# Optimization experiments

Hardware: AMD Instinct MI355X
Metric: run time of the kernel (lower is better)

## Reference

```python
import jax, jax.numpy as jnp
import numpy as np

BN_EPS = 1e-5


def setup_inputs() -> dict:
    key = jax.random.key(0)
    ks = jax.random.split(key, 10)
    N, C, T, V, S, IC = 128, 64, 288, 16, 3, 16
    x = jax.random.normal(ks[0], (N, C, T, V), dtype=jnp.float32)
    A_base = jax.random.uniform(ks[1], (S, V, V), dtype=jnp.float32)
    PA = jax.random.normal(ks[2], (S, V, V), dtype=jnp.float32) * 1e-3
    Wa = jax.random.normal(ks[3], (S, IC, C), dtype=jnp.float32) * 0.1
    ba = jax.random.normal(ks[4], (S, IC), dtype=jnp.float32) * 0.1
    Wb = jax.random.normal(ks[5], (S, IC, C), dtype=jnp.float32) * 0.1
    bb = jax.random.normal(ks[6], (S, IC), dtype=jnp.float32) * 0.1
    Wd = jax.random.normal(ks[7], (S, C, C), dtype=jnp.float32) * 0.1
    bd = jax.random.normal(ks[8], (S, C), dtype=jnp.float32) * 0.1
    gamma = jnp.ones((C,), dtype=jnp.float32)
    beta = jnp.zeros((C,), dtype=jnp.float32)
    return {"x": x, "A_base": A_base, "PA": PA, "Wa": Wa, "ba": ba,
            "Wb": Wb, "bb": bb, "Wd": Wd, "bd": bd,
            "gamma": gamma, "beta": beta}


def reference(x, A_base, PA, Wa, ba, Wb, bb, Wd, bd, gamma, beta):
    N, C, T, V = x.shape
    S, IC, _ = Wa.shape
    A = A_base + PA  # [s,v,w]
    # 1x1 convs for all subsets at once: [n,s,ic,t,v]
    fa = jnp.einsum('nctv,sic->nsitv', x, Wa) + ba[None, :, :, None, None]
    fb = jnp.einsum('nctv,sic->nsitv', x, Wb) + bb[None, :, :, None, None]
    # A1: permute(0,3,1,2).view(N,V,IC*T) -> [n,s,v,(ic*t)]
    A1 = fa.transpose(0, 1, 4, 2, 3).reshape(N, S, V, IC * T)
    # A2: view(N, IC*T, V) -> [n,s,(ic*t),v]
    A2 = fb.reshape(N, S, IC * T, V)
    att = jnp.einsum('nsvk,nskw->nsvw', A1, A2) / float(IC * T)
    att = jax.nn.softmax(att, axis=2)  # torch softmax(dim=1) on [N,V,V]
    att = att + A[None]  # [n,s,v,w]
    # x.view(N,C*T,V) @ att, per subset: [n,s,c,t,w]
    z = jnp.einsum('nctv,nsvw->nsctw', x, att)
    # conv_d per subset then sum over subsets
    y = jnp.einsum('nsctw,soc->notw', z, Wd) + bd.sum(0)[None, :, None, None]
    # inference BN (running mean 0, var 1)
    scale = gamma / jnp.sqrt(1.0 + BN_EPS)
    y = y * scale[None, :, None, None] + beta[None, :, None, None]
    # residual (in_channels == out_channels -> identity down path)
    return y + x
```

## Files before the change

kernel.cpp:

```cpp
#include <hip/hip_runtime.h>
#include <math.h>

#define NN 128
#define CC 64
#define TT 288
#define VV 16
#define SS 3
#define ICC 16

#define SLICES 12
#define TSL (TT / SLICES)
#define CHUNKS (TSL / 8)

#define OTB 16

typedef __attribute__((ext_vector_type(8))) short s16x8;
typedef __attribute__((ext_vector_type(4))) float f32x4;

#define MFMA16(a, b, c) __builtin_amdgcn_mfma_f32_16x16x32_bf16(a, b, c, 0, 0, 0)

__device__ __forceinline__ unsigned short f2bf(float f) {
    union { float f; unsigned u; } x; x.f = f;
    unsigned r = (x.u + 0x7FFFu + ((x.u >> 16) & 1u)) >> 16;
    return (unsigned short)r;
}

__device__ __forceinline__ unsigned cvt2bf(float lo, float hi) {
    unsigned r;
    asm("v_cvt_pk_bf16_f32 %0, %1, %2" : "=v"(r) : "v"(lo), "v"(hi));
    return r;
}

__device__ __forceinline__ s16x8 zero8() {
    s16x8 z;
#pragma unroll
    for (int j = 0; j < 8; ++j) z[j] = 0;
    return z;
}

__device__ __forceinline__ s16x8 cvt8g(const float* p) {
    float4 a = *(const float4*)p;
    float4 b = *(const float4*)(p + 4);
    union { unsigned u[4]; s16x8 v; } r;
    r.u[0] = cvt2bf(a.x, a.y); r.u[1] = cvt2bf(a.z, a.w);
    r.u[2] = cvt2bf(b.x, b.y); r.u[3] = cvt2bf(b.z, b.w);
    return r.v;
}

__device__ __forceinline__ int xaddr(int col, int c) {
    int chunk = ((c >> 3) ^ (col & 7) ^ ((col >> 3) & 7)) & 7;
    return col * 64 + chunk * 8 + (c & 7);
}
__device__ __forceinline__ int xaddr16(int col, int ck) {
    int chunk = (ck ^ (col & 7) ^ ((col >> 3) & 7)) & 7;
    return col * 64 + chunk * 8;
}

__global__ void k_prep(const float* __restrict__ bd, const float* __restrict__ gamma,
                       const float* __restrict__ beta, const float* __restrict__ Wd,
                       float* __restrict__ cmul, float* __restrict__ cadd,
                       unsigned short* __restrict__ wd_bf) {
    const int tid = threadIdx.x;
    if (blockIdx.x == 0 && tid < CC) {
        float mul = gamma[tid] * rsqrtf(1.0f + 1e-5f);
        float add = (bd[tid] + bd[CC + tid] + bd[2 * CC + tid]) * mul + beta[tid];
        cmul[tid] = mul;
        cadd[tid] = add;
    }
    for (int e = blockIdx.x * 256 + tid; e < SS * CC * CC; e += 16 * 256)
        wd_bf[e] = f2bf(Wd[e]);
}

__global__ __launch_bounds__(256) void k_logits(
    const float* __restrict__ x,
    const float* __restrict__ Wa, const float* __restrict__ ba,
    const float* __restrict__ Wb, const float* __restrict__ bb,
    float* __restrict__ part)
{
    const int b    = blockIdx.x;
    const int n    = b / SLICES;
    const int sl   = b % SLICES;
    const int tid  = threadIdx.x;
    const int lane = tid & 63;
    const int wave = tid >> 6;
    const int q    = lane >> 4;
    const int m    = lane & 15;

    __shared__ __align__(16) unsigned short xsb[128 * 64];
    __shared__ __align__(16) unsigned short fa_l[SS][16][136];
    __shared__ __align__(16) unsigned short fb_l[SS][16][136];

    s16x8 wa[SS][2], wb[SS][2];
    float4 ba_r[SS], bb_r[SS];
#pragma unroll
    for (int s = 0; s < SS; ++s) {
#pragma unroll
        for (int kt = 0; kt < 2; ++kt) {
            wa[s][kt] = cvt8g(Wa + ((size_t)(s * ICC + m) * CC + kt * 32 + q * 8));
            wb[s][kt] = cvt8g(Wb + ((size_t)(s * ICC + m) * CC + kt * 32 + q * 8));
        }
        ba_r[s] = *(const float4*)(ba + s * ICC + q * 4);
        bb_r[s] = *(const float4*)(bb + s * ICC + q * 4);
    }

    f32x4 accL[SS];
#pragma unroll
    for (int s = 0; s < SS; ++s)
#pragma unroll
        for (int r = 0; r < 4; ++r) accL[s][r] = 0.0f;

    const float* xn = x + (size_t)n * CC * TT * VV;
    const int tbase = sl * TSL;

    float4 px[8];
#pragma unroll
    for (int i = 0; i < 8; ++i) {
        int f4 = tid + i * 256;
        int c = f4 >> 5, col4 = (f4 & 31) * 4;
        px[i] = *(const float4*)(xn + (size_t)c * (TT * VV) + (size_t)tbase * VV + col4);
    }

#pragma unroll
    for (int ch = 0; ch < CHUNKS; ++ch) {
        __syncthreads();
#pragma unroll
        for (int i = 0; i < 8; ++i) {
            int f4 = tid + i * 256;
            int c = f4 >> 5, col4 = (f4 & 31) * 4;
            unsigned s01 = cvt2bf(px[i].x, px[i].y);
            unsigned s23 = cvt2bf(px[i].z, px[i].w);
            xsb[xaddr(col4 + 0, c)] = (unsigned short)(s01 & 0xffff);
            xsb[xaddr(col4 + 1, c)] = (unsigned short)(s01 >> 16);
            xsb[xaddr(col4 + 2, c)] = (unsigned short)(s23 & 0xffff);
            xsb[xaddr(col4 + 3, c)] = (unsigned short)(s23 >> 16);
        }
        __syncthreads();

        s16x8 bx[2][2];
#pragma unroll
        for (int tli = 0; tli < 2; ++tli) {
            int col = (wave * 2 + tli) * 16 + m;
#pragma unroll
            for (int kt = 0; kt < 2; ++kt)
                bx[tli][kt] = *(const s16x8*)&xsb[xaddr16(col, kt * 4 + q)];
        }

        if (ch + 1 < CHUNKS) {
#pragma unroll
            for (int i = 0; i < 8; ++i) {
                int f4 = tid + i * 256;
                int c = f4 >> 5, col4 = (f4 & 31) * 4;
                px[i] = *(const float4*)(xn + (size_t)c * (TT * VV) +
                                         (size_t)(tbase + (ch + 1) * 8) * VV + col4);
            }
        }

#pragma unroll
        for (int s = 0; s < SS; ++s) {
#pragma unroll
            for (int tli = 0; tli < 2; ++tli) {
                const int tl = wave * 2 + tli;
                f32x4 aa, ab;
                aa[0] = ba_r[s].x; aa[1] = ba_r[s].y; aa[2] = ba_r[s].z; aa[3] = ba_r[s].w;
                ab[0] = bb_r[s].x; ab[1] = bb_r[s].y; ab[2] = bb_r[s].z; ab[3] = bb_r[s].w;
#pragma unroll
                for (int kt = 0; kt < 2; ++kt) {
                    aa = MFMA16(wa[s][kt], bx[tli][kt], aa);
                    ab = MFMA16(wb[s][kt], bx[tli][kt], ab);
                }
                uint2 ua, ub;
                ua.x = cvt2bf(aa[0], aa[1]); ua.y = cvt2bf(aa[2], aa[3]);
                ub.x = cvt2bf(ab[0], ab[1]); ub.y = cvt2bf(ab[2], ab[3]);
                *reinterpret_cast<uint2*>(&fa_l[s][m][tl * 16 + 4 * q]) = ua;
                *reinterpret_cast<uint2*>(&fb_l[s][m][tl * 16 + 4 * q]) = ub;
            }
            s16x8 A2 = *(const s16x8*)&fa_l[s][m][wave * 32 + q * 8];
            s16x8 B2 = *(const s16x8*)&fb_l[s][m][wave * 32 + q * 8];
            accL[s] = MFMA16(A2, B2, accL[s]);
        }
    }

    __syncthreads();
    float* red = (float*)xsb;
#pragma unroll
    for (int s = 0; s < SS; ++s)
#pragma unroll
        for (int r = 0; r < 4; ++r)
            red[(s * 4 + wave) * 256 + (4 * q + r) * 16 + m] = accL[s][r];
    __syncthreads();
#pragma unroll
    for (int s = 0; s < SS; ++s) {
        float v = red[(s * 4 + 0) * 256 + tid] + red[(s * 4 + 1) * 256 + tid] +
                  red[(s * 4 + 2) * 256 + tid] + red[(s * 4 + 3) * 256 + tid];
        part[((size_t)(sl * NN + n) * SS + s) * 256 + tid] = v;
    }
}

__global__ __launch_bounds__(256) void k_softmax(
    const float* __restrict__ part,
    const float* __restrict__ A_base, const float* __restrict__ PA,
    float* __restrict__ att)
{
    const int n = blockIdx.x / SS;
    const int s = blockIdx.x % SS;
    const int tid = threadIdx.x;
    const int w = tid & 15;

    __shared__ float l[256];
    size_t base = ((size_t)n * SS + s) * 256;
    float mine = 0.0f;
#pragma unroll
    for (int p = 0; p < SLICES; ++p)
        mine += part[(size_t)p * (NN * SS * 256) + base + tid];
    mine *= (1.0f / (ICC * TT));
    l[tid] = mine;
    __syncthreads();

    float mx = -1e30f;
#pragma unroll
    for (int v2 = 0; v2 < 16; ++v2) mx = fmaxf(mx, l[v2 * 16 + w]);
    float sm = 0.f;
#pragma unroll
    for (int v2 = 0; v2 < 16; ++v2) sm += __expf(l[v2 * 16 + w] - mx);
    float r = __expf(mine - mx) / sm;

    int aidx = (s * VV * VV) + tid;
    att[base + tid] = r + A_base[aidx] + PA[aidx];
}

__global__ __launch_bounds__(256) void k_out(
    const float* __restrict__ x, const float* __restrict__ att,
    const unsigned short* __restrict__ wd_bf,
    const float* __restrict__ cmul, const float* __restrict__ cadd,
    float* __restrict__ out)
{
    const int b  = blockIdx.x;
    const int n  = b / (TT / OTB);
    const int t0 = (b % (TT / OTB)) * OTB;

    const int tid  = threadIdx.x;
    const int lane = tid & 63;
    const int wave = tid >> 6;
    const int q    = lane >> 4;
    const int m    = lane & 15;

    __shared__ __align__(16) unsigned char uni[36864];
    __shared__ __align__(16) unsigned short attL[SS][16][24];

    unsigned short* xsb = (unsigned short*)uni;
    unsigned short* zsb = (unsigned short*)uni;
    float*          osb = (float*)uni;

    {
        const float* xrow0 = x + ((size_t)(n * CC) * TT + t0) * VV;
#pragma unroll
        for (int i = 0; i < 16; ++i) {
            int c = wave * 16 + i;
            float4 f = *(const float4*)(xrow0 + (size_t)c * (TT * VV) + lane * 4);
            uint2 u2; u2.x = cvt2bf(f.x, f.y); u2.y = cvt2bf(f.z, f.w);
            int tcol  = lane * 4;
            int chunk = (tcol >> 3) ^ (c & 7);
            *(uint2*)&xsb[c * 256 + chunk * 8 + (tcol & 7)] = u2;
        }
    }
    for (int e = tid; e < SS * 256; e += 256) {
        int ss = e >> 8, vv = (e >> 4) & 15, ww = e & 15;
        attL[ss][ww][vv] = f2bf(att[((size_t)n * SS + ss) * 256 + vv * 16 + ww]);
    }

    __syncthreads();

    s16x8 xf[4][4];
#pragma unroll
    for (int cc = 0; cc < 4; ++cc)
#pragma unroll
        for (int u = 0; u < 4; ++u) {
            s16x8 f = zero8();
            if (q < 2) {
                int c = cc * 16 + m;
                int chunk = ((4 * wave + u) * 2 + q) ^ (c & 7);
                f = *(const s16x8*)&xsb[c * 256 + chunk * 8];
            }
            xf[cc][u] = f;
        }

    __syncthreads();

    f32x4 acc[4][4];
#pragma unroll
    for (int p = 0; p < 4; ++p)
#pragma unroll
        for (int u = 0; u < 4; ++u)
#pragma unroll
            for (int r = 0; r < 4; ++r) acc[p][u][r] = 0.0f;

#pragma unroll
    for (int s = 0; s < SS; ++s) {
        s16x8 af = zero8();
        if (q < 2) af = *(const s16x8*)&attL[s][m][q * 8];

#pragma unroll
        for (int u = 0; u < 4; ++u)
#pragma unroll
            for (int cc = 0; cc < 4; ++cc) {
                f32x4 z;
#pragma unroll
                for (int r = 0; r < 4; ++r) z[r] = 0.0f;
                z = MFMA16(xf[cc][u], af, z);
                uint2 uz; uz.x = cvt2bf(z[0], z[1]); uz.y = cvt2bf(z[2], z[3]);
                *(uint2*)&zsb[((wave * 64) + u * 16 + m) * 72 + cc * 16 + 4 * q] = uz;
            }

        s16x8 zf[4][2];
#pragma unroll
        for (int u = 0; u < 4; ++u)
#pragma unroll
            for (int kt = 0; kt < 2; ++kt)
                zf[u][kt] = *(const s16x8*)&zsb[((wave * 64) + u * 16 + m) * 72 +
                                                kt * 32 + q * 8];

#pragma unroll
        for (int p = 0; p < 4; ++p) {
            s16x8 wf[2];
#pragma unroll
            for (int kt = 0; kt < 2; ++kt)
                wf[kt] = *(const s16x8*)(wd_bf +
                           ((size_t)(s * CC + p * 16 + m) * CC + kt * 32 + q * 8));
#pragma unroll
            for (int u = 0; u < 4; ++u)
#pragma unroll
                for (int kt = 0; kt < 2; ++kt)
                    acc[p][u] = MFMA16(wf[kt], zf[u][kt], acc[p][u]);
        }
    }

#pragma unroll
    for (int p = 0; p < 4; ++p) {
        float4 mu = *(const float4*)(cmul + p * 16 + 4 * q);
        float4 ad = *(const float4*)(cadd + p * 16 + 4 * q);
        float mur[4] = {mu.x, mu.y, mu.z, mu.w};
        float adr[4] = {ad.x, ad.y, ad.z, ad.w};
#pragma unroll
        for (int u = 0; u < 4; ++u)
#pragma unroll
            for (int r = 0; r < 4; ++r)
                acc[p][u][r] = acc[p][u][r] * mur[r] + adr[r];
    }

#pragma unroll
    for (int hp = 0; hp < 2; ++hp) {
        __syncthreads();
#pragma unroll
        for (int pp = 0; pp < 2; ++pp)
#pragma unroll
            for (int u = 0; u < 4; ++u)
#pragma unroll
                for (int r = 0; r < 4; ++r)
                    osb[(pp * 16 + 4 * q + r) * 268 + (4 * wave + u) * 16 + m] =
                        acc[hp * 2 + pp][u][r];
        __syncthreads();
#pragma unroll
        for (int j = 0; j < 8; ++j) {
            int orow = wave * 8 + j;
            int o = hp * 32 + orow;
            float4 v = *(const float4*)&osb[orow * 268 + lane * 4];
            size_t off = ((size_t)(n * CC + o) * TT + t0) * VV + lane * 4;
            float4 xr = *(const float4*)(x + off);
            float4 res;
            res.x = v.x + xr.x; res.y = v.y + xr.y;
            res.z = v.z + xr.z; res.w = v.w + xr.w;
            *(float4*)(out + off) = res;
        }
    }
}

extern "C" void kernel_launch(void* const* d_in, const int* in_sizes, int n_in,
                              void* d_out, int out_size, void* d_ws, size_t ws_size,
                              hipStream_t stream) {
    const float* x      = (const float*)d_in[0];
    const float* A_base = (const float*)d_in[1];
    const float* PA     = (const float*)d_in[2];
    const float* Wa     = (const float*)d_in[3];
    const float* ba     = (const float*)d_in[4];
    const float* Wb     = (const float*)d_in[5];
    const float* bb     = (const float*)d_in[6];
    const float* Wd     = (const float*)d_in[7];
    const float* bd     = (const float*)d_in[8];
    const float* gamma  = (const float*)d_in[9];
    const float* beta   = (const float*)d_in[10];
    float* out = (float*)d_out;

    float* part = (float*)d_ws;
    float* att  = part;
    float* cmul = part + (size_t)SLICES * NN * SS * 256;
    float* cadd = cmul + CC;
    unsigned short* wd_bf = (unsigned short*)(cadd + CC);

    k_prep<<<16, 256, 0, stream>>>(bd, gamma, beta, Wd, cmul, cadd, wd_bf);
    k_logits<<<NN * SLICES, 256, 0, stream>>>(x, Wa, ba, Wb, bb, part);
    k_softmax<<<NN * SS, 256, 0, stream>>>(part, A_base, PA, att);
    k_out<<<NN * (TT / OTB), 256, 0, stream>>>(x, att, wd_bf, cmul, cadd, out);
}
```

Measured before the change: 351.9 us.

## Halve output time tile and write k_out results directly with residual from LDS

Shrinks the k_out time tile from 16 to 8 steps, which doubles the number of blocks and halves the per-wave register tiles. xsb and zsb now get separate LDS buffers, so one barrier goes away. The fp32 LDS staging of the output and the second global read of x are dropped. Each lane now writes its MFMA accumulators straight to global memory as scalar stores, adding the residual from the bf16 copy of x held in LDS. This cuts LDS round-trips and global reads, but the stores become narrower and less coalesced, and the residual add now uses bf16-rounded x, which lowers accuracy.

```diff
diff --git a/kernel.cpp b/kernel.cpp
--- a/kernel.cpp
+++ b/kernel.cpp
@@ -12,7 +12,7 @@
 #define TSL (TT / SLICES)
 #define CHUNKS (TSL / 8)
 
-#define OTB 16
+#define OTB 8
 
 typedef __attribute__((ext_vector_type(8))) short s16x8;
 typedef __attribute__((ext_vector_type(4))) float f32x4;
@@ -244,23 +244,21 @@
     const int q    = lane >> 4;
     const int m    = lane & 15;
 
-    __shared__ __align__(16) unsigned char uni[36864];
+    __shared__ __align__(16) unsigned short xsb[64 * 128];
+    __shared__ __align__(16) unsigned short zsb[4 * 32 * 72];
     __shared__ __align__(16) unsigned short attL[SS][16][24];
-
-    unsigned short* xsb = (unsigned short*)uni;
-    unsigned short* zsb = (unsigned short*)uni;
-    float*          osb = (float*)uni;
 
     {
         const float* xrow0 = x + ((size_t)(n * CC) * TT + t0) * VV;
 #pragma unroll
-        for (int i = 0; i < 16; ++i) {
-            int c = wave * 16 + i;
-            float4 f = *(const float4*)(xrow0 + (size_t)c * (TT * VV) + lane * 4);
+        for (int i = 0; i < 8; ++i) {
+            int f4   = tid + i * 256;
+            int c    = f4 >> 5;
+            int col4 = (f4 & 31) * 4;
+            float4 f = *(const float4*)(xrow0 + (size_t)c * (TT * VV) + col4);
             uint2 u2; u2.x = cvt2bf(f.x, f.y); u2.y = cvt2bf(f.z, f.w);
-            int tcol  = lane * 4;
-            int chunk = (tcol >> 3) ^ (c & 7);
-            *(uint2*)&xsb[c * 256 + chunk * 8 + (tcol & 7)] = u2;
+            int chunk = (col4 >> 3) ^ (c & 7);
+            *(uint2*)&xsb[c * 128 + chunk * 8 + (col4 & 7)] = u2;
         }
     }
     for (int e = tid; e < SS * 256; e += 256) {
@@ -270,27 +268,26 @@
 
     __syncthreads();
 
-    s16x8 xf[4][4];
+    s16x8 xf[4][2];
 #pragma unroll
     for (int cc = 0; cc < 4; ++cc)
 #pragma unroll
-        for (int u = 0; u < 4; ++u) {
+        for (int u = 0; u < 2; ++u) {
             s16x8 f = zero8();
             if (q < 2) {
                 int c = cc * 16 + m;
-                int chunk = ((4 * wave + u) * 2 + q) ^ (c & 7);
-                f = *(const s16x8*)&xsb[c * 256 + chunk * 8];
+                int t = wave * 2 + u;
+                int chunk = (2 * t + q) ^ (c & 7);
+                f = *(const s16x8*)&xsb[c * 128 + chunk * 8];
             }
             xf[cc][u] = f;
         }
 
-    __syncthreads();
-
-    f32x4 acc[4][4];
+    f32x4 acc[4][2];
 #pragma unroll
     for (int p = 0; p < 4; ++p)
 #pragma unroll
-        for (int u = 0; u < 4; ++u)
+        for (int u = 0; u < 2; ++u)
 #pragma unroll
             for (int r = 0; r < 4; ++r) acc[p][u][r] = 0.0f;
 
@@ -300,7 +297,7 @@
         if (q < 2) af = *(const s16x8*)&attL[s][m][q * 8];
 
 #pragma unroll
-        for (int u = 0; u < 4; ++u)
+        for (int u = 0; u < 2; ++u)
 #pragma unroll
             for (int cc = 0; cc < 4; ++cc) {
                 f32x4 z;
@@ -308,15 +305,15 @@
                 for (int r = 0; r < 4; ++r) z[r] = 0.0f;
                 z = MFMA16(xf[cc][u], af, z);
                 uint2 uz; uz.x = cvt2bf(z[0], z[1]); uz.y = cvt2bf(z[2], z[3]);
-                *(uint2*)&zsb[((wave * 64) + u * 16 + m) * 72 + cc * 16 + 4 * q] = uz;
-            }
-
-        s16x8 zf[4][2];
-#pragma unroll
-        for (int u = 0; u < 4; ++u)
+                *(uint2*)&zsb[(wave * 32 + u * 16 + m) * 72 + cc * 16 + 4 * q] = uz;
+            }
+
+        s16x8 zf[2][2];
+#pragma unroll
+        for (int u = 0; u < 2; ++u)
 #pragma unroll
             for (int kt = 0; kt < 2; ++kt)
-                zf[u][kt] = *(const s16x8*)&zsb[((wave * 64) + u * 16 + m) * 72 +
+                zf[u][kt] = *(const s16x8*)&zsb[(wave * 32 + u * 16 + m) * 72 +
                                                 kt * 32 + q * 8];
 
 #pragma unroll
@@ -327,13 +324,14 @@
                 wf[kt] = *(const s16x8*)(wd_bf +
                            ((size_t)(s * CC + p * 16 + m) * CC + kt * 32 + q * 8));
 #pragma unroll
-            for (int u = 0; u < 4; ++u)
+            for (int u = 0; u < 2; ++u)
 #pragma unroll
                 for (int kt = 0; kt < 2; ++kt)
                     acc[p][u] = MFMA16(wf[kt], zf[u][kt], acc[p][u]);
         }
     }
 
+    const size_t obase = ((size_t)(n * CC) * TT + t0) * VV;
 #pragma unroll
     for (int p = 0; p < 4; ++p) {
         float4 mu = *(const float4*)(cmul + p * 16 + 4 * q);
@@ -341,35 +339,18 @@
         float mur[4] = {mu.x, mu.y, mu.z, mu.w};
         float adr[4] = {ad.x, ad.y, ad.z, ad.w};
 #pragma unroll
-        for (int u = 0; u < 4; ++u)
-#pragma unroll
-            for (int r = 0; r < 4; ++r)
-                acc[p][u][r] = acc[p][u][r] * mur[r] + adr[r];
-    }
-
-#pragma unroll
-    for (int hp = 0; hp < 2; ++hp) {
-        __syncthreads();
-#pragma unroll
-        for (int pp = 0; pp < 2; ++pp)
-#pragma unroll
-            for (int u = 0; u < 4; ++u)
-#pragma unroll
-                for (int r = 0; r < 4; ++r)
-                    osb[(pp * 16 + 4 * q + r) * 268 + (4 * wave + u) * 16 + m] =
-                        acc[hp * 2 + pp][u][r];
-        __syncthreads();
-#pragma unroll
-        for (int j = 0; j < 8; ++j) {
-            int orow = wave * 8 + j;
-            int o = hp * 32 + orow;
-            float4 v = *(const float4*)&osb[orow * 268 + lane * 4];
-            size_t off = ((size_t)(n * CC + o) * TT + t0) * VV + lane * 4;
-            float4 xr = *(const float4*)(x + off);
-            float4 res;
-            res.x = v.x + xr.x; res.y = v.y + xr.y;
-            res.z = v.z + xr.z; res.w = v.w + xr.w;
-            *(float4*)(out + off) = res;
+        for (int u = 0; u < 2; ++u) {
+            int tl   = wave * 2 + u;
+            int tcol = tl * 16 + m;
+#pragma unroll
+            for (int r = 0; r < 4; ++r) {
+                int o = p * 16 + 4 * q + r;
+                int chunk = (tcol >> 3) ^ (o & 7);
+                unsigned xb = xsb[o * 128 + chunk * 8 + (tcol & 7)];
+                union { unsigned u32; float f; } cv; cv.u32 = xb << 16;
+                out[obase + (size_t)o * (TT * VV) + tl * VV + m] =
+                    acc[p][u][r] * mur[r] + adr[r] + cv.f;
+            }
         }
     }
 }
```

Result: slower. 361.8 us (+2.8%).
